# Kernel tuning notes

Hardware: AMD Instinct MI355X
Metric: run time of the kernel (lower is better)

Reference implementation:

```python
import jax, jax.numpy as jnp
import numpy as np

N_NODES = 20000
N_EDGES = 256000
F_IN = 1024
HID = 1000
N_CLS = 1000
NEG_SLOPE = 0.2


def _glorot(key, shape):
    fan_in, fan_out = shape[1], shape[0]
    lim = np.sqrt(6.0 / (fan_in + fan_out))
    return jax.random.uniform(key, shape, jnp.float32, -lim, lim)


def setup_inputs() -> dict:
    key = jax.random.key(0)
    ks = jax.random.split(key, 16)
    x = jax.random.normal(ks[0], (N_NODES, F_IN), jnp.float32)
    edge_index = jax.random.randint(ks[1], (2, N_EDGES), 0, N_NODES, jnp.int64)
    edge_attr = jax.random.uniform(ks[2], (N_EDGES, 1), jnp.float32)
    return {
        "x": x,
        "edge_index": edge_index,
        "edge_attr": edge_attr,
        # conv1 params (GATv2Conv: F_IN -> HID, heads=1, edge_dim=1)
        "w1_l": _glorot(ks[3], (HID, F_IN)),
        "b1_l": jnp.zeros((HID,), jnp.float32),
        "w1_r": _glorot(ks[4], (HID, F_IN)),
        "b1_r": jnp.zeros((HID,), jnp.float32),
        "w1_e": _glorot(ks[5], (HID, 1)),
        "att1": _glorot(ks[6], (1, HID))[0],
        "bias1": jnp.zeros((HID,), jnp.float32),
        # conv2 params (HID -> N_CLS, heads=1, concat=False)
        "w2_l": _glorot(ks[7], (N_CLS, HID)),
        "b2_l": jnp.zeros((N_CLS,), jnp.float32),
        "w2_r": _glorot(ks[8], (N_CLS, HID)),
        "b2_r": jnp.zeros((N_CLS,), jnp.float32),
        "w2_e": _glorot(ks[9], (N_CLS, 1)),
        "att2": _glorot(ks[10], (1, N_CLS))[0],
        "bias2": jnp.zeros((N_CLS,), jnp.float32),
    }


def gatv2_layer(x, src, dst, edge_attr, Wl, bl, Wr, br, We, att, bias):
    # GATv2Conv with heads=1 (eval mode: attention dropout inactive).
    n = x.shape[0]
    xl = x @ Wl.T + bl                       # source-side transform [N, C]
    xr = x @ Wr.T + br                       # target-side transform [N, C]
    e = xl[src] + xr[dst] + edge_attr @ We.T  # per-edge features [E, C]
    e = jax.nn.leaky_relu(e, NEG_SLOPE)
    logits = e @ att                          # [E]
    # segment softmax over incoming edges of each target node
    m = jax.ops.segment_max(logits, dst, num_segments=n)
    alpha = jnp.exp(logits - m[dst])
    denom = jax.ops.segment_sum(alpha, dst, num_segments=n)
    alpha = alpha / (denom[dst] + 1e-16)
    out = jax.ops.segment_sum(xl[src] * alpha[:, None], dst, num_segments=n)
    return out + bias


def reference(x, edge_index, edge_attr,
              w1_l, b1_l, w1_r, b1_r, w1_e, att1, bias1,
              w2_l, b2_l, w2_r, b2_r, w2_e, att2, bias2):
    src, dst = edge_index[0], edge_index[1]
    # feature dropout (p=0.6) is identity in eval mode
    h = gatv2_layer(x, src, dst, edge_attr, w1_l, b1_l, w1_r, b1_r, w1_e, att1, bias1)
    h = jax.nn.relu(h)
    h = gatv2_layer(h, src, dst, edge_attr, w2_l, b2_l, w2_r, b2_r, w2_e, att2, bias2)
    return jax.nn.sigmoid(h)
```

## Files before the change

### kernel.cpp

```cpp
#include <hip/hip_runtime.h>
#include <math.h>

#define N_NODES 20000
#define N_EDGES 256000
#define F_IN 1024
#define C_DIM 1000
#define NEG_SLOPE 0.2f

#define MPAD 20096
#define KDIM 1024
#define NW 2048

typedef __attribute__((ext_vector_type(8))) short          bf16x8;
typedef __attribute__((ext_vector_type(8))) unsigned short u16x8;
typedef __attribute__((ext_vector_type(4))) float          f32x4;
typedef unsigned short us;

__device__ __forceinline__ us f2bf(float f) {
  unsigned u = __float_as_uint(f);
  return (us)((u + 0x7FFFu + ((u >> 16) & 1u)) >> 16);
}
__device__ __forceinline__ float bf2f(us u) {
  return __uint_as_float(((unsigned)u) << 16);
}

__device__ __forceinline__ void gld16(void* lds, const void* g) {
  __builtin_amdgcn_global_load_lds(
      (const __attribute__((address_space(1))) unsigned int*)g,
      (__attribute__((address_space(3))) unsigned int*)lds, 16, 0, 0);
}

__global__ void count_k(const int* __restrict__ edst, int* __restrict__ counts) {
  int e = blockIdx.x * blockDim.x + threadIdx.x;
  if (e < N_EDGES) atomicAdd(&counts[edst[e]], 1);
}

__global__ __launch_bounds__(1024)
void scan_k(const int* __restrict__ counts, int* __restrict__ row_ptr, int* __restrict__ cursor) {
  __shared__ int sm[1024];
  int t = threadIdx.x;
  int base = t * 20;
  int loc[20];
  int run = 0;
#pragma unroll
  for (int i = 0; i < 20; ++i) {
    int idx = base + i;
    int v = (idx < N_NODES) ? counts[idx] : 0;
    run += v;
    loc[i] = run;
  }
  sm[t] = run;
  __syncthreads();
  for (int off = 1; off < 1024; off <<= 1) {
    int v = (t >= off) ? sm[t - off] : 0;
    __syncthreads();
    sm[t] += v;
    __syncthreads();
  }
  int excl = (t > 0) ? sm[t - 1] : 0;
#pragma unroll
  for (int i = 0; i < 20; ++i) {
    int idx = base + i;
    if (idx < N_NODES) {
      int e = excl + ((i > 0) ? loc[i - 1] : 0);
      row_ptr[idx] = e;
      cursor[idx] = e;
    }
  }
  if (t == 0) row_ptr[N_NODES] = sm[1023];
}

__global__ void scatter_k(const int* __restrict__ esrc, const float* __restrict__ eattr,
                          const int* __restrict__ edst, int* __restrict__ cursor,
                          int2* __restrict__ spair) {
  int e = blockIdx.x * blockDim.x + threadIdx.x;
  if (e < N_EDGES) {
    int p = atomicAdd(&cursor[edst[e]], 1);
    spair[p] = make_int2(esrc[e], __float_as_int(eattr[e]));
  }
}

__global__ void cvt_pad_k(const float* __restrict__ src, us* __restrict__ dst,
                          int R, int C, int dstRows) {
  long total = (long)dstRows * 256;
  for (long i = (long)blockIdx.x * blockDim.x + threadIdx.x; i < total;
       i += (long)gridDim.x * blockDim.x) {
    int row = (int)(i >> 8);
    int c = ((int)(i & 255)) << 2;
    ushort4 o = make_ushort4(0, 0, 0, 0);
    if (row < R && c < C) {
      float4 v = *(const float4*)(src + (long)row * C + c);
      o.x = f2bf(v.x); o.y = f2bf(v.y); o.z = f2bf(v.z); o.w = f2bf(v.w);
    }
    *(ushort4*)(dst + ((long)row << 10) + c) = o;
  }
}

__global__ __launch_bounds__(256)
void gemm_mfma_k(const us* __restrict__ Abf, const us* __restrict__ Wbf,
                 const float* __restrict__ bl, const float* __restrict__ br,
                 us* __restrict__ Cbf) {
  __shared__ us As0[4096], As1[4096], Bs0[4096], Bs1[4096];
  const int tid = threadIdx.x;
  const int lane = tid & 63;
  const int wv = tid >> 6;
  const int wr = wv >> 1, wc = wv & 1;

  const int nwg = gridDim.x;
  const int q = nwg >> 3;
  const int wg = (blockIdx.x & 7) * q + (blockIdx.x >> 3);
  const long bm = (long)(wg >> 4) * 128;
  const long bn = (long)(wg & 15) * 128;

  f32x4 acc[4][4];
  const f32x4 z4 = {0.f, 0.f, 0.f, 0.f};
#pragma unroll
  for (int i = 0; i < 4; ++i)
#pragma unroll
    for (int j = 0; j < 4; ++j) acc[i][j] = z4;

  const int i0 = tid, i1 = tid + 256;
  const us* gA0 = Abf + (bm + (i0 >> 2)) * KDIM + (i0 & 3) * 8;
  const us* gA1 = Abf + (bm + (i1 >> 2)) * KDIM + (i1 & 3) * 8;
  const us* gB0 = Wbf + (bn + (i0 >> 2)) * KDIM + (i0 & 3) * 8;
  const us* gB1 = Wbf + (bn + (i1 >> 2)) * KDIM + (i1 & 3) * 8;

  const int g = lane >> 4;
  const int rA = lane & 15;

  gld16(As0 + wv * 512, gA0);
  gld16(As0 + 2048 + wv * 512, gA1);
  gld16(Bs0 + wv * 512, gB0);
  gld16(Bs0 + 2048 + wv * 512, gB1);
  __syncthreads();

  for (int t = 0; t < 32; ++t) {
    if (t + 1 < 32) {
      int kn = (t + 1) << 5;
      us* dA = ((t + 1) & 1) ? As1 : As0;
      us* dB = ((t + 1) & 1) ? Bs1 : Bs0;
      gld16(dA + wv * 512, gA0 + kn);
      gld16(dA + 2048 + wv * 512, gA1 + kn);
      gld16(dB + wv * 512, gB0 + kn);
      gld16(dB + 2048 + wv * 512, gB1 + kn);
    }
    const us* Ar = (t & 1) ? As1 : As0;
    const us* Br = (t & 1) ? Bs1 : Bs0;
    bf16x8 av[4], bv[4];
#pragma unroll
    for (int mi = 0; mi < 4; ++mi)
      av[mi] = *(const bf16x8*)&Ar[(wr * 64 + mi * 16 + rA) * 32 + g * 8];
#pragma unroll
    for (int ni = 0; ni < 4; ++ni)
      bv[ni] = *(const bf16x8*)&Br[(wc * 64 + ni * 16 + rA) * 32 + g * 8];
#pragma unroll
    for (int mi = 0; mi < 4; ++mi)
#pragma unroll
      for (int ni = 0; ni < 4; ++ni)
        acc[mi][ni] = __builtin_amdgcn_mfma_f32_16x16x32_bf16(av[mi], bv[ni], acc[mi][ni], 0, 0, 0);
    __syncthreads();
  }

  int coln[4]; float biasv[4]; int cok[4];
#pragma unroll
  for (int ni = 0; ni < 4; ++ni) {
    coln[ni] = (int)bn + wc * 64 + ni * 16 + rA;
    int cm = coln[ni] & 1023;
    cok[ni] = (cm < C_DIM);
    biasv[ni] = cok[ni] ? ((coln[ni] < 1024) ? bl[cm] : br[cm]) : 0.f;
  }
#pragma unroll
  for (int mi = 0; mi < 4; ++mi) {
#pragma unroll
    for (int j = 0; j < 4; ++j) {
      int row = (int)bm + wr * 64 + mi * 16 + g * 4 + j;
      if (row < N_NODES) {
#pragma unroll
        for (int ni = 0; ni < 4; ++ni)
          if (cok[ni])
            Cbf[(long)row * NW + coln[ni]] = f2bf(acc[mi][ni][j] + biasv[ni]);
      }
    }
  }
}

template <int ACT>
__global__ __launch_bounds__(256)
void edge_agg_k(const us* __restrict__ xlr, const int2* __restrict__ spair,
                const int* __restrict__ row_ptr,
                const float* __restrict__ We, const float* __restrict__ att,
                const float* __restrict__ bias, us* __restrict__ hout,
                float* __restrict__ fout) {
  const int wave = threadIdx.x >> 6;
  const int lane = threadIdx.x & 63;
  const int q0 = lane, q1 = lane + 64;
  const bool ok1 = (q1 < 125);

  float attv[2][8], wev[2][8];
#pragma unroll
  for (int j = 0; j < 2; ++j) {
    int qq = lane + 64 * j;
    if (qq < 125) {
      float4 a0 = ((const float4*)att)[2 * qq], a1 = ((const float4*)att)[2 * qq + 1];
      float4 w0 = ((const float4*)We)[2 * qq],  w1 = ((const float4*)We)[2 * qq + 1];
      attv[j][0] = a0.x; attv[j][1] = a0.y; attv[j][2] = a0.z; attv[j][3] = a0.w;
      attv[j][4] = a1.x; attv[j][5] = a1.y; attv[j][6] = a1.z; attv[j][7] = a1.w;
      wev[j][0] = w0.x; wev[j][1] = w0.y; wev[j][2] = w0.z; wev[j][3] = w0.w;
      wev[j][4] = w1.x; wev[j][5] = w1.y; wev[j][6] = w1.z; wev[j][7] = w1.w;
    } else {
#pragma unroll
      for (int t = 0; t < 8; ++t) { attv[j][t] = 0.f; wev[j][t] = 0.f; }
    }
  }

  const int gw = (blockIdx.x << 2) | wave;
  const int stride = gridDim.x << 2;

  for (int d = gw; d < N_NODES; d += stride) {
    const int beg = row_ptr[d];
    const int end = row_ptr[d + 1];

    float xrv[2][8];
    {
      const u16x8* xrp = (const u16x8*)(xlr + (long)d * NW + 1024);
#pragma unroll
      for (int j = 0; j < 2; ++j) {
        int qq = lane + 64 * j;
        if (qq < 125) {
          u16x8 h = xrp[qq];
#pragma unroll
          for (int t = 0; t < 8; ++t) xrv[j][t] = bf2f(h[t]);
        } else {
#pragma unroll
          for (int t = 0; t < 8; ++t) xrv[j][t] = 0.f;
        }
      }
    }

    float m = -INFINITY, denom = 0.f;
    float acc[2][8];
#pragma unroll
    for (int j = 0; j < 2; ++j)
#pragma unroll
      for (int t = 0; t < 8; ++t) acc[j][t] = 0.f;

#define EDGE_LOGIT(PAIR, VH0, VH1, PART)                                   \
    {                                                                      \
      const u16x8* xs = (const u16x8*)(xlr + (long)(PAIR).x * NW);         \
      float ea = __int_as_float((PAIR).y);                                 \
      VH0 = xs[q0];                                                        \
      if (ok1) VH1 = xs[q1];                                               \
      else { u16x8 zz = {0,0,0,0,0,0,0,0}; VH1 = zz; }                     \
      PART = 0.f;                                                          \
      _Pragma("unroll")                                                    \
      for (int t = 0; t < 8; ++t) {                                        \
        float tt = bf2f(VH0[t]) + xrv[0][t] + ea * wev[0][t];              \
        tt = (tt >= 0.f) ? tt : NEG_SLOPE * tt;                            \
        PART = fmaf(attv[0][t], tt, PART);                                 \
        float uu = bf2f(VH1[t]) + xrv[1][t] + ea * wev[1][t];              \
        uu = (uu >= 0.f) ? uu : NEG_SLOPE * uu;                            \
        PART = fmaf(attv[1][t], uu, PART);                                 \
      }                                                                    \
    }

#define ONLINE_UPDATE(PART, VH0, VH1)                                      \
    {                                                                      \
      if ((PART) > m) {                                                    \
        float sc = __expf(m - (PART));                                     \
        denom = denom * sc + 1.f;                                          \
        _Pragma("unroll")                                                  \
        for (int t = 0; t < 8; ++t) {                                      \
          acc[0][t] = fmaf(acc[0][t], sc, bf2f(VH0[t]));                   \
          acc[1][t] = fmaf(acc[1][t], sc, bf2f(VH1[t]));                   \
        }                                                                  \
        m = (PART);                                                        \
      } else {                                                             \
        float w = __expf((PART) - m);                                      \
        denom += w;                                                        \
        _Pragma("unroll")                                                  \
        for (int t = 0; t < 8; ++t) {                                      \
          acc[0][t] = fmaf(w, bf2f(VH0[t]), acc[0][t]);                    \
          acc[1][t] = fmaf(w, bf2f(VH1[t]), acc[1][t]);                    \
        }                                                                  \
      }                                                                    \
    }

    int i = beg;
    for (; i + 2 <= end; i += 2) {
      int2 p0 = spair[i], p1 = spair[i + 1];
      u16x8 a0, a1, b0, b1;
      float part0, part1;
      EDGE_LOGIT(p0, a0, a1, part0);
      EDGE_LOGIT(p1, b0, b1, part1);
#pragma unroll
      for (int off = 32; off > 0; off >>= 1) {
        part0 += __shfl_xor(part0, off, 64);
        part1 += __shfl_xor(part1, off, 64);
      }
      ONLINE_UPDATE(part0, a0, a1);
      ONLINE_UPDATE(part1, b0, b1);
    }
    if (i < end) {
      int2 p0 = spair[i];
      u16x8 a0, a1;
      float part0;
      EDGE_LOGIT(p0, a0, a1, part0);
#pragma unroll
      for (int off = 32; off > 0; off >>= 1) part0 += __shfl_xor(part0, off, 64);
      ONLINE_UPDATE(part0, a0, a1);
    }
#undef EDGE_LOGIT
#undef ONLINE_UPDATE

    float inv = 1.f / (denom + 1e-16f);
    if (ACT == 0) {
      us* orow = hout + ((long)d << 10);
#pragma unroll
      for (int j = 0; j < 2; ++j) {
        int qq = lane + 64 * j;
        u16x8 pk = {0, 0, 0, 0, 0, 0, 0, 0};
        if (qq < 125) {
          const float4 b0 = ((const float4*)bias)[2 * qq], b1 = ((const float4*)bias)[2 * qq + 1];
          const float bb[8] = {b0.x, b0.y, b0.z, b0.w, b1.x, b1.y, b1.z, b1.w};
#pragma unroll
          for (int t = 0; t < 8; ++t)
            pk[t] = f2bf(fmaxf(fmaf(acc[j][t], inv, bb[t]), 0.f));
        }
        ((u16x8*)orow)[qq] = pk;
      }
    } else {
#pragma unroll
      for (int j = 0; j < 2; ++j) {
        int qq = lane + 64 * j;
        if (qq < 125) {
          const float4 b0 = ((const float4*)bias)[2 * qq], b1 = ((const float4*)bias)[2 * qq + 1];
          const float bb[8] = {b0.x, b0.y, b0.z, b0.w, b1.x, b1.y, b1.z, b1.w};
          float o[8];
#pragma unroll
          for (int t = 0; t < 8; ++t)
            o[t] = 1.f / (1.f + __expf(-fmaf(acc[j][t], inv, bb[t])));
          float4* op = (float4*)(fout + (long)d * C_DIM + 8 * qq);
          op[0] = make_float4(o[0], o[1], o[2], o[3]);
          op[1] = make_float4(o[4], o[5], o[6], o[7]);
        }
      }
    }
  }
}

extern "C" void kernel_launch(void* const* d_in, const int* in_sizes, int n_in,
                              void* d_out, int out_size, void* d_ws, size_t ws_size,
                              hipStream_t stream) {
  const float* x     = (const float*)d_in[0];
  const int*   ei    = (const int*)d_in[1];
  const float* eattr = (const float*)d_in[2];
  const float* w1l   = (const float*)d_in[3];
  const float* b1l   = (const float*)d_in[4];
  const float* w1r   = (const float*)d_in[5];
  const float* b1r   = (const float*)d_in[6];
  const float* w1e   = (const float*)d_in[7];
  const float* att1  = (const float*)d_in[8];
  const float* bias1 = (const float*)d_in[9];
  const float* w2l   = (const float*)d_in[10];
  const float* b2l   = (const float*)d_in[11];
  const float* w2r   = (const float*)d_in[12];
  const float* b2r   = (const float*)d_in[13];
  const float* w2e   = (const float*)d_in[14];
  const float* att2  = (const float*)d_in[15];
  const float* bias2 = (const float*)d_in[16];
  float* out = (float*)d_out;

  char* w = (char*)d_ws;
  us*  xlr  = (us*)w;
  us*  Abf  = (us*)(w + 82313216L);
  us*  W2   = (us*)(w + 123469824L);
  int2* spair = (int2*)(w + 127664128L);
  int* row_ptr = (int*)(w + 129712128L);
  int* cursor  = row_ptr + (N_NODES + 1);
  int* counts  = cursor + N_NODES;

  const int* esrc = ei;
  const int* edst = ei + N_EDGES;

  hipMemsetAsync(counts, 0, N_NODES * sizeof(int), stream);
  count_k<<<(N_EDGES + 255) / 256, 256, 0, stream>>>(edst, counts);
  scan_k<<<1, 1024, 0, stream>>>(counts, row_ptr, cursor);
  scatter_k<<<(N_EDGES + 255) / 256, 256, 0, stream>>>(esrc, eattr, edst, cursor, spair);

  cvt_pad_k<<<4096, 256, 0, stream>>>(x, Abf, N_NODES, F_IN, MPAD);
  cvt_pad_k<<<1024, 256, 0, stream>>>(w1l, W2, C_DIM, F_IN, 1024);
  cvt_pad_k<<<1024, 256, 0, stream>>>(w1r, W2 + 1024 * 1024, C_DIM, F_IN, 1024);
  gemm_mfma_k<<<2512, 256, 0, stream>>>(Abf, W2, b1l, b1r, xlr);
  edge_agg_k<0><<<2048, 256, 0, stream>>>(xlr, spair, row_ptr, w1e, att1, bias1, Abf, nullptr);

  cvt_pad_k<<<1024, 256, 0, stream>>>(w2l, W2, C_DIM, C_DIM, 1024);
  cvt_pad_k<<<1024, 256, 0, stream>>>(w2r, W2 + 1024 * 1024, C_DIM, C_DIM, 1024);
  gemm_mfma_k<<<2512, 256, 0, stream>>>(Abf, W2, b2l, b2r, xlr);
  edge_agg_k<1><<<2048, 256, 0, stream>>>(xlr, spair, row_ptr, w2e, att2, bias2, nullptr, out);
}
```

Measured before the change: 521.5 us.

## Enlarge GEMM tiles with swizzled LDS and dynamic node queue in edge aggregation

The GEMM kernel moves to 512-thread blocks with 128x256 tiles and a 64-wide K step. LDS is laid out with an XOR swizzle to avoid bank conflicts, and the grouped block-index remap is dropped. The edge aggregation kernels now pull destination nodes from an atomic work queue instead of a static grid stride, to balance the uneven in-degree per node. Workspace offsets and MPAD change to fit the larger tiles, and the memset now also clears the queue counters. The tradeoff is more LDS per block, which can lower occupancy, plus atomic traffic per node.

```diff
diff --git a/kernel.cpp b/kernel.cpp
--- a/kernel.cpp
+++ b/kernel.cpp
@@ -7,7 +7,7 @@
 #define C_DIM 1000
 #define NEG_SLOPE 0.2f
 
-#define MPAD 20096
+#define MPAD 20224
 #define KDIM 1024
 #define NW 2048
 
@@ -96,21 +96,20 @@
   }
 }
 
-__global__ __launch_bounds__(256)
+__global__ __launch_bounds__(512)
 void gemm_mfma_k(const us* __restrict__ Abf, const us* __restrict__ Wbf,
                  const float* __restrict__ bl, const float* __restrict__ br,
                  us* __restrict__ Cbf) {
-  __shared__ us As0[4096], As1[4096], Bs0[4096], Bs1[4096];
+  __shared__ us As[2][8192];
+  __shared__ us Bs[2][16384];
   const int tid = threadIdx.x;
   const int lane = tid & 63;
   const int wv = tid >> 6;
-  const int wr = wv >> 1, wc = wv & 1;
-
-  const int nwg = gridDim.x;
-  const int q = nwg >> 3;
-  const int wg = (blockIdx.x & 7) * q + (blockIdx.x >> 3);
-  const long bm = (long)(wg >> 4) * 128;
-  const long bn = (long)(wg & 15) * 128;
+  const int wr = wv >> 2;
+  const int wc = wv & 3;
+
+  const long bm = (long)(blockIdx.x >> 3) * 128;
+  const long bn = (long)(blockIdx.x & 7) * 256;
 
   f32x4 acc[4][4];
   const f32x4 z4 = {0.f, 0.f, 0.f, 0.f};
@@ -119,55 +118,73 @@
 #pragma unroll
     for (int j = 0; j < 4; ++j) acc[i][j] = z4;
 
-  const int i0 = tid, i1 = tid + 256;
-  const us* gA0 = Abf + (bm + (i0 >> 2)) * KDIM + (i0 & 3) * 8;
-  const us* gA1 = Abf + (bm + (i1 >> 2)) * KDIM + (i1 & 3) * 8;
-  const us* gB0 = Wbf + (bn + (i0 >> 2)) * KDIM + (i0 & 3) * 8;
-  const us* gB1 = Wbf + (bn + (i1 >> 2)) * KDIM + (i1 & 3) * 8;
-
+  const us* srcA[2];
+  const us* srcB[4];
+#pragma unroll
+  for (int r = 0; r < 2; ++r) {
+    int c = tid + r * 512;
+    int row = c >> 3;
+    int kc = (c & 7) ^ (row & 7);
+    srcA[r] = Abf + (bm + row) * KDIM + kc * 8;
+  }
+#pragma unroll
+  for (int r = 0; r < 4; ++r) {
+    int c = tid + r * 512;
+    int row = c >> 3;
+    int kc = (c & 7) ^ (row & 7);
+    srcB[r] = Wbf + (bn + row) * KDIM + kc * 8;
+  }
+
+#define STAGE(buf, k0)                                          \
+  {                                                             \
+    _Pragma("unroll")                                           \
+    for (int r = 0; r < 2; ++r)                                 \
+      gld16(&As[buf][r * 4096 + wv * 512], srcA[r] + (k0));     \
+    _Pragma("unroll")                                           \
+    for (int r = 0; r < 4; ++r)                                 \
+      gld16(&Bs[buf][r * 4096 + wv * 512], srcB[r] + (k0));     \
+  }
+
+  const int rA = lane & 15;
   const int g = lane >> 4;
-  const int rA = lane & 15;
-
-  gld16(As0 + wv * 512, gA0);
-  gld16(As0 + 2048 + wv * 512, gA1);
-  gld16(Bs0 + wv * 512, gB0);
-  gld16(Bs0 + 2048 + wv * 512, gB1);
-  __syncthreads();
-
-  for (int t = 0; t < 32; ++t) {
-    if (t + 1 < 32) {
-      int kn = (t + 1) << 5;
-      us* dA = ((t + 1) & 1) ? As1 : As0;
-      us* dB = ((t + 1) & 1) ? Bs1 : Bs0;
-      gld16(dA + wv * 512, gA0 + kn);
-      gld16(dA + 2048 + wv * 512, gA1 + kn);
-      gld16(dB + wv * 512, gB0 + kn);
-      gld16(dB + 2048 + wv * 512, gB1 + kn);
-    }
-    const us* Ar = (t & 1) ? As1 : As0;
-    const us* Br = (t & 1) ? Bs1 : Bs0;
-    bf16x8 av[4], bv[4];
-#pragma unroll
-    for (int mi = 0; mi < 4; ++mi)
-      av[mi] = *(const bf16x8*)&Ar[(wr * 64 + mi * 16 + rA) * 32 + g * 8];
-#pragma unroll
-    for (int ni = 0; ni < 4; ++ni)
-      bv[ni] = *(const bf16x8*)&Br[(wc * 64 + ni * 16 + rA) * 32 + g * 8];
-#pragma unroll
-    for (int mi = 0; mi < 4; ++mi)
+  const int kb0 = ((g) ^ (rA & 7)) * 8;
+  const int kb1 = ((4 + g) ^ (rA & 7)) * 8;
+  const int arow = (wr * 64 + rA) * 64;
+  const int brow = (wc * 64 + rA) * 64;
+
+  STAGE(0, 0)
+
+  for (int t = 0; t < 16; ++t) {
+    __syncthreads();
+    if (t < 15) STAGE((t + 1) & 1, (t + 1) * 64)
+    const us* Ar = As[t & 1];
+    const us* Br = Bs[t & 1];
+#pragma unroll
+    for (int ks = 0; ks < 2; ++ks) {
+      const int kb = ks ? kb1 : kb0;
+      bf16x8 bv[4];
 #pragma unroll
       for (int ni = 0; ni < 4; ++ni)
-        acc[mi][ni] = __builtin_amdgcn_mfma_f32_16x16x32_bf16(av[mi], bv[ni], acc[mi][ni], 0, 0, 0);
-    __syncthreads();
-  }
-
-  int coln[4]; float biasv[4]; int cok[4];
+        bv[ni] = *(const bf16x8*)&Br[brow + ni * 1024 + kb];
+      bf16x8 av[4];
+#pragma unroll
+      for (int mi = 0; mi < 4; ++mi)
+        av[mi] = *(const bf16x8*)&Ar[arow + mi * 1024 + kb];
+#pragma unroll
+      for (int mi = 0; mi < 4; ++mi)
+#pragma unroll
+        for (int ni = 0; ni < 4; ++ni)
+          acc[mi][ni] = __builtin_amdgcn_mfma_f32_16x16x32_bf16(av[mi], bv[ni], acc[mi][ni], 0, 0, 0);
+    }
+  }
+
+  int coln[4]; float bsv[4]; int cok[4];
 #pragma unroll
   for (int ni = 0; ni < 4; ++ni) {
     coln[ni] = (int)bn + wc * 64 + ni * 16 + rA;
     int cm = coln[ni] & 1023;
     cok[ni] = (cm < C_DIM);
-    biasv[ni] = cok[ni] ? ((coln[ni] < 1024) ? bl[cm] : br[cm]) : 0.f;
+    bsv[ni] = cok[ni] ? ((coln[ni] < 1024) ? bl[cm] : br[cm]) : 0.f;
   }
 #pragma unroll
   for (int mi = 0; mi < 4; ++mi) {
@@ -178,20 +195,20 @@
 #pragma unroll
         for (int ni = 0; ni < 4; ++ni)
           if (cok[ni])
-            Cbf[(long)row * NW + coln[ni]] = f2bf(acc[mi][ni][j] + biasv[ni]);
+            Cbf[(long)row * NW + coln[ni]] = f2bf(acc[mi][ni][j] + bsv[ni]);
       }
     }
   }
+#undef STAGE
 }
 
 template <int ACT>
 __global__ __launch_bounds__(256)
 void edge_agg_k(const us* __restrict__ xlr, const int2* __restrict__ spair,
-                const int* __restrict__ row_ptr,
+                const int* __restrict__ row_ptr, int* __restrict__ qctr,
                 const float* __restrict__ We, const float* __restrict__ att,
                 const float* __restrict__ bias, us* __restrict__ hout,
                 float* __restrict__ fout) {
-  const int wave = threadIdx.x >> 6;
   const int lane = threadIdx.x & 63;
   const int q0 = lane, q1 = lane + 64;
   const bool ok1 = (q1 < 125);
@@ -213,10 +230,11 @@
     }
   }
 
-  const int gw = (blockIdx.x << 2) | wave;
-  const int stride = gridDim.x << 2;
-
-  for (int d = gw; d < N_NODES; d += stride) {
+  int d;
+  if (lane == 0) d = atomicAdd(qctr, 1);
+  d = __shfl(d, 0, 64);
+
+  while (d < N_NODES) {
     const int beg = row_ptr[d];
     const int end = row_ptr[d + 1];
 
@@ -345,6 +363,9 @@
         }
       }
     }
+
+    if (lane == 0) d = atomicAdd(qctr, 1);
+    d = __shfl(d, 0, 64);
   }
 }
 
@@ -372,17 +393,18 @@
 
   char* w = (char*)d_ws;
   us*  xlr  = (us*)w;
-  us*  Abf  = (us*)(w + 82313216L);
-  us*  W2   = (us*)(w + 123469824L);
-  int2* spair = (int2*)(w + 127664128L);
-  int* row_ptr = (int*)(w + 129712128L);
+  us*  Abf  = (us*)(w + 81920000L);
+  us*  W2   = (us*)(w + 123338752L);
+  int2* spair = (int2*)(w + 127533056L);
+  int* row_ptr = (int*)(w + 129581056L);
   int* cursor  = row_ptr + (N_NODES + 1);
   int* counts  = cursor + N_NODES;
+  int* qctr    = counts + N_NODES;
 
   const int* esrc = ei;
   const int* edst = ei + N_EDGES;
 
-  hipMemsetAsync(counts, 0, N_NODES * sizeof(int), stream);
+  hipMemsetAsync(counts, 0, (N_NODES + 2) * sizeof(int), stream);
   count_k<<<(N_EDGES + 255) / 256, 256, 0, stream>>>(edst, counts);
   scan_k<<<1, 1024, 0, stream>>>(counts, row_ptr, cursor);
   scatter_k<<<(N_EDGES + 255) / 256, 256, 0, stream>>>(esrc, eattr, edst, cursor, spair);
@@ -390,11 +412,13 @@
   cvt_pad_k<<<4096, 256, 0, stream>>>(x, Abf, N_NODES, F_IN, MPAD);
   cvt_pad_k<<<1024, 256, 0, stream>>>(w1l, W2, C_DIM, F_IN, 1024);
   cvt_pad_k<<<1024, 256, 0, stream>>>(w1r, W2 + 1024 * 1024, C_DIM, F_IN, 1024);
-  gemm_mfma_k<<<2512, 256, 0, stream>>>(Abf, W2, b1l, b1r, xlr);
-  edge_agg_k<0><<<2048, 256, 0, stream>>>(xlr, spair, row_ptr, w1e, att1, bias1, Abf, nullptr);
+  gemm_mfma_k<<<1264, 512, 0, stream>>>(Abf, W2, b1l, b1r, xlr);
+  edge_agg_k<0><<<1024, 256, 0, stream>>>(xlr, spair, row_ptr, qctr, w1e, att1, bias1,
+                                          Abf, nullptr);
 
   cvt_pad_k<<<1024, 256, 0, stream>>>(w2l, W2, C_DIM, C_DIM, 1024);
   cvt_pad_k<<<1024, 256, 0, stream>>>(w2r, W2 + 1024 * 1024, C_DIM, C_DIM, 1024);
-  gemm_mfma_k<<<2512, 256, 0, stream>>>(Abf, W2, b2l, b2r, xlr);
-  edge_agg_k<1><<<2048, 256, 0, stream>>>(xlr, spair, row_ptr, w2e, att2, bias2, nullptr, out);
-}
+  gemm_mfma_k<<<1264, 512, 0, stream>>>(Abf, W2, b2l, b2r, xlr);
+  edge_agg_k<1><<<1024, 256, 0, stream>>>(xlr, spair, row_ptr, qctr + 1, w2e, att2, bias2,
+                                          nullptr, out);
+}
```

Result: slower. 975.8 us (+87.1%).
